# Optimization experiments

Measured on AMD Instinct MI355X. Metric: run time of the kernel, lower is better.

The kernel has to match this reference:

```python
import jax, jax.numpy as jnp
import numpy as np

N_QUBITS = 6
N_LAYERS = 2
QSVT_DEGREE = 3
DT_RANK = max(N_QUBITS // 2, 1)
OUT_DIM = 3 * N_QUBITS
PI = np.float32(np.pi)
DT_MIN, DT_MAX = 1e-3, 0.1
BATCH, SEQ = 256, 512


def _ry_mat(theta):
    c = jnp.cos(theta / 2)
    s = jnp.sin(theta / 2)
    row0 = jnp.stack([c, -s], axis=-1)
    row1 = jnp.stack([s, c], axis=-1)
    return jnp.stack([row0, row1], axis=-2).astype(jnp.complex64)


def _rz_mat(theta):
    e = jnp.exp(-0.5j * theta.astype(jnp.complex64))
    z = jnp.zeros_like(e)
    row0 = jnp.stack([e, z], axis=-1)
    row1 = jnp.stack([z, jnp.conj(e)], axis=-1)
    return jnp.stack([row0, row1], axis=-2)


def _rx_mat(theta):
    c = jnp.cos(theta / 2).astype(jnp.complex64)
    s = jnp.sin(theta / 2).astype(jnp.complex64)
    row0 = jnp.stack([c, -1j * s], axis=-1)
    row1 = jnp.stack([-1j * s, c], axis=-1)
    return jnp.stack([row0, row1], axis=-2)


def _apply1(state, mat, w):
    # state: (B, 2, ..., 2) tensor over N_QUBITS axes; mat: (2,2) or batched (B,2,2)
    state = jnp.moveaxis(state, 1 + w, -1)
    if mat.ndim == 3:
        state = jnp.einsum('bij,b...j->b...i', mat, state)
    else:
        state = jnp.einsum('ij,b...j->b...i', mat, state)
    return jnp.moveaxis(state, -1, 1 + w)


def _cnot(state, c, t):
    state = jnp.moveaxis(state, (1 + c, 1 + t), (-2, -1))
    state = state.at[..., 1, :].set(state[..., 1, ::-1])
    return jnp.moveaxis(state, (-2, -1), (1 + c, 1 + t))


def _crx(state, theta, c, t):
    state = jnp.moveaxis(state, (1 + c, 1 + t), (-2, -1))
    m = _rx_mat(theta)
    state = state.at[..., 1, :].set(jnp.einsum('ij,...j->...i', m, state[..., 1, :]))
    return jnp.moveaxis(state, (-2, -1), (1 + c, 1 + t))


def _circuit(h, x, dt, circuit_params, poly_coeffs, qsvt_params):
    """Batched statevector simulation of the selective QSVT + unified ansatz qnode."""
    n = N_QUBITS
    B = h.shape[0]
    state = jnp.zeros((B,) + (2,) * n, jnp.complex64)
    state = state.at[(slice(None),) + (0,) * n].set(1.0 + 0.0j)
    # 1) state encoding RY(h[t-1])
    for i in range(n):
        state = _apply1(state, _ry_mat(h[:, i]), i)
    # 2) Delta-modulated QSVT: RZ rotations + bidirectional CNOT ring per degree
    qidx = 0
    n_qp = n * QSVT_DEGREE
    for deg in range(QSVT_DEGREE + 1):
        coeff = poly_coeffs[deg]
        for i in range(n):
            if qidx < n_qp:
                ang = coeff * dt[:, i] * qsvt_params[qidx] * PI
                qidx += 1
            else:
                ang = coeff * dt[:, i] * PI
            state = _apply1(state, _rz_mat(ang), i)
        for i in range(n - 1):
            state = _cnot(state, i, i + 1)
        state = _cnot(state, n - 1, 0)
        for i in range(n - 1, 0, -1):
            state = _cnot(state, i, i - 1)
    # 3) unified variational ansatz
    p = 0
    for _ in range(N_LAYERS):
        for i in range(n):
            state = _apply1(state, _rx_mat(circuit_params[p]), i)
            state = _apply1(state, _ry_mat(circuit_params[p + 1]), i)
            state = _apply1(state, _rz_mat(circuit_params[p + 2]), i)
            p += 3
        for i in range(n):
            state = _crx(state, circuit_params[p], i, (i + 1) % n)
            p += 1
        for i in range(n - 1, -1, -1):
            state = _crx(state, circuit_params[p], i, (i - 1) % n)
            p += 1
    # 4) Delta-modulated input RY(x * dt)
    for i in range(n):
        state = _apply1(state, _ry_mat(x[:, i] * dt[:, i]), i)
    # 5) Pauli X/Y/Z expectation values per qubit
    xs, ys, zs = [], [], []
    for i in range(n):
        s = jnp.moveaxis(state, 1 + i, 1).reshape(B, 2, -1)
        z = jnp.sum(jnp.conj(s[:, 0]) * s[:, 1], axis=-1)
        xs.append(2.0 * jnp.real(z))
        ys.append(2.0 * jnp.imag(z))
        zs.append(jnp.sum(jnp.abs(s[:, 0]) ** 2 - jnp.abs(s[:, 1]) ** 2, axis=-1))
    return jnp.stack(xs + ys + zs, axis=-1).astype(jnp.float32)  # (B, 3n)


def setup_inputs() -> dict:
    key = jax.random.key(0)
    ks = jax.random.split(key, 8)
    angles = jax.random.uniform(ks[0], (BATCH, SEQ, N_QUBITS), jnp.float32) * PI
    Wx = jax.random.normal(ks[1], (DT_RANK + 2 * N_QUBITS, N_QUBITS), jnp.float32) / np.float32(np.sqrt(N_QUBITS))
    Wdt = jax.random.normal(ks[2], (N_QUBITS, DT_RANK), jnp.float32) / np.float32(np.sqrt(DT_RANK))
    dt = jnp.exp(jax.random.uniform(ks[3], (N_QUBITS,), jnp.float32) * np.float32(np.log(DT_MAX) - np.log(DT_MIN)) + np.float32(np.log(DT_MIN)))
    bdt = dt + jnp.log(-jnp.expm1(-dt))
    poly_coeffs = jax.random.normal(ks[4], (QSVT_DEGREE + 1,), jnp.float32) * 0.1
    qsvt_params = jax.random.normal(ks[5], (N_QUBITS * QSVT_DEGREE,), jnp.float32) * 0.1
    circuit_params = jax.random.normal(ks[6], (5 * N_QUBITS * N_LAYERS,), jnp.float32) * 0.1
    D = jnp.ones((OUT_DIM,), jnp.float32)
    Wc = jax.random.normal(ks[7], (OUT_DIM, N_QUBITS), jnp.float32) / np.float32(np.sqrt(N_QUBITS))
    return {"angles": angles, "Wx": Wx, "Wdt": Wdt, "bdt": bdt, "poly_coeffs": poly_coeffs, "qsvt_params": qsvt_params, "circuit_params": circuit_params, "D": D, "Wc": Wc}


def reference(angles, Wx, Wdt, bdt, poly_coeffs, qsvt_params, circuit_params, D, Wc):
    x_dbc = angles @ Wx.T  # (B,S, dt_rank + 2n)
    dt_raw = x_dbc[..., :DT_RANK]
    # B slice computed in the original but never used in forward
    C = x_dbc[..., DT_RANK + N_QUBITS:]
    dt_angles = jnp.tanh(jax.nn.softplus(dt_raw @ Wdt.T + bdt)) * PI  # (B,S,n)
    # quantum part is detached in the original (detach().cpu() before the qnode)
    sg = jax.lax.stop_gradient
    xs = (jnp.moveaxis(sg(angles), 1, 0), jnp.moveaxis(sg(dt_angles), 1, 0))
    cp, pc, qp = sg(circuit_params), sg(poly_coeffs), sg(qsvt_params)
    h0 = jnp.zeros((angles.shape[0], N_QUBITS), jnp.float32)

    def step(h, xt):
        x_t, dt_t = xt
        meas = _circuit(h, x_t, dt_t, cp, pc, qp)
        return meas[:, 2 * N_QUBITS:], meas  # carry = PauliZ block

    _, meas = jax.lax.scan(step, h0, xs)
    h_full = jnp.moveaxis(meas, 0, 1)  # (B,S,3n)
    return (C @ Wc.T) * h_full + D * jnp.concatenate([angles] * 3, axis=-1)
```

## Files before the change

kernel.cpp:

```cpp
#include <hip/hip_runtime.h>
#include <math.h>

#define BATCH 256
#define SEQ 512
#define SDS 54
#define PI_F 3.14159265358979323846f

template<int CTRL>
__device__ __forceinline__ float fdpp(float v) {
    return __int_as_float(__builtin_amdgcn_mov_dpp(__float_as_int(v), CTRL, 0xF, 0xF, true));
}
template<int L>
__device__ __forceinline__ float rdl(float v) {
    return __int_as_float(__builtin_amdgcn_readlane(__float_as_int(v), L));
}
__device__ __forceinline__ float rdlv(float v, int l) {
    return __int_as_float(__builtin_amdgcn_readlane(__float_as_int(v), l));
}
template<int M>
__device__ __forceinline__ float shxm(float v) {
    if constexpr (M == 1)       return fdpp<0xB1>(v);
    else if constexpr (M == 2)  return fdpp<0x4E>(v);
    else if constexpr (M == 8)  return fdpp<0x128>(v);
    else if constexpr (M == 32) return __shfl_xor(v, 32, 64);
    else return __int_as_float(__builtin_amdgcn_ds_swizzle(__float_as_int(v), (M << 10) | 0x1F));
}
__device__ __forceinline__ float redsum64(float v) {
    v += fdpp<0x128>(v);
    v += fdpp<0x124>(v);
    v += fdpp<0x122>(v);
    v += fdpp<0x121>(v);
    return (rdl<0>(v) + rdl<16>(v)) + (rdl<32>(v) + rdl<48>(v));
}
__device__ __forceinline__ float xorf(float v, int m) {
    return __int_as_float(__float_as_int(v) ^ m);
}
__device__ __forceinline__ void wg_barrier_lds() {
    __builtin_amdgcn_sched_barrier(0);
    __builtin_amdgcn_s_waitcnt(0xC07F);
    __builtin_amdgcn_s_barrier();
    __builtin_amdgcn_sched_barrier(0);
}
__device__ __forceinline__ int permf(int x) {
    const int cs[11] = {0,1,2,3,4,5,5,4,3,2,1};
    const int ts[11] = {1,2,3,4,5,0,4,3,2,1,0};
#pragma unroll
    for (int k = 10; k >= 0; k--) {
        int cb = (x >> (5 - cs[k])) & 1;
        x ^= cb << (5 - ts[k]);
    }
    return x;
}
__device__ __forceinline__ void cmul4(const float* c,
    float vr, float vi, float ar, float ai, float br, float bi, float cr, float ci,
    float& nr, float& ni) {
    nr = c[0]*vr - c[1]*vi + c[2]*ar - c[3]*ai + c[4]*br - c[5]*bi + c[6]*cr - c[7]*ci;
    ni = c[0]*vi + c[1]*vr + c[2]*ai + c[3]*ar + c[4]*bi + c[5]*br + c[6]*ci + c[7]*cr;
}
__device__ __forceinline__ void ringapply(const float* rc,
    float vr, float vi, float br, float bi, float cr, float ci, float dr, float di,
    float& nr, float& ni) {
    nr = rc[0]*vr - rc[1]*bi - rc[2]*ci + rc[3]*dr;
    ni = rc[0]*vi + rc[1]*br + rc[2]*cr + rc[3]*di;
}

__global__ __launch_bounds__(256) void prep_kernel(
    const float* __restrict__ angles, const float* __restrict__ Wx,
    const float* __restrict__ Wdt, const float* __restrict__ bdt,
    const float* __restrict__ D, const float* __restrict__ Wc,
    float* __restrict__ sd)
{
    int gid = blockIdx.x * blockDim.x + threadIdx.x;
    if (gid >= BATCH * SEQ) return;
    const float* a = angles + (size_t)gid * 6;
    float ang[6];
#pragma unroll
    for (int i = 0; i < 6; i++) ang[i] = a[i];
    float dtr[3];
#pragma unroll
    for (int r = 0; r < 3; r++) {
        float s = 0.f;
#pragma unroll
        for (int k = 0; k < 6; k++) s += ang[k] * Wx[r * 6 + k];
        dtr[r] = s;
    }
    float* rec = sd + (size_t)gid * SDS;
    float dtv[6];
#pragma unroll
    for (int i = 0; i < 6; i++) {
        float x = bdt[i];
#pragma unroll
        for (int r = 0; r < 3; r++) x += dtr[r] * Wdt[i * 3 + r];
        float sp = (x > 15.f) ? x : log1pf(expf(x));
        dtv[i] = tanhf(sp) * PI_F;
        rec[i] = dtv[i];
        float th = ang[i] * dtv[i];
        rec[6 + i]  = cosf(th);
        rec[12 + i] = sinf(th);
    }
    float C[6];
#pragma unroll
    for (int i = 0; i < 6; i++) {
        float s = 0.f;
#pragma unroll
        for (int k = 0; k < 6; k++) s += ang[k] * Wx[(9 + i) * 6 + k];
        C[i] = s;
    }
#pragma unroll
    for (int j = 0; j < 18; j++) {
        float s = 0.f;
#pragma unroll
        for (int i = 0; i < 6; i++) s += C[i] * Wc[j * 6 + i];
        rec[18 + j] = s;
        rec[36 + j] = D[j] * ang[j % 6];
    }
}

__global__ __launch_bounds__(64) void umat_kernel(const float* __restrict__ cp,
                                                  float2* __restrict__ um)
{
    const int lane = threadIdx.x;
    const int col = blockIdx.x;
    int bitv[6];
#pragma unroll
    for (int i = 0; i < 6; i++) bitv[i] = (lane >> (5 - i)) & 1;

    float qc[2][3][8], rc[2][6][4];
#pragma unroll
    for (int l = 0; l < 2; l++) {
        float g00r[6], g00i[6], g01r[6], g01i[6], g10r[6], g10i[6], g11r[6], g11i[6];
#pragma unroll
        for (int i = 0; i < 6; i++) {
            float ax = cp[l * 30 + i * 3 + 0];
            float ay = cp[l * 30 + i * 3 + 1];
            float az = cp[l * 30 + i * 3 + 2];
            float ca = cosf(0.5f * ax), sa = sinf(0.5f * ax);
            float cb = cosf(0.5f * ay), sb = sinf(0.5f * ay);
            float cg = cosf(0.5f * az), sg = sinf(0.5f * az);
            float m00r = cb * ca, m00i =  sb * sa;
            float m01r = -sb * ca, m01i = -cb * sa;
            float m10r =  sb * ca, m10i = -cb * sa;
            float m11r =  cb * ca, m11i = -sb * sa;
            g00r[i] = cg * m00r + sg * m00i; g00i[i] = cg * m00i - sg * m00r;
            g01r[i] = cg * m01r + sg * m01i; g01i[i] = cg * m01i - sg * m01r;
            g10r[i] = cg * m10r - sg * m10i; g10i[i] = cg * m10i + sg * m10r;
            g11r[i] = cg * m11r - sg * m11i; g11i[i] = cg * m11i + sg * m11r;
        }
#pragma unroll
        for (int pp = 0; pp < 3; pp++) {
            int aq = 2 * pp, bq = 2 * pp + 1;
            float dar = bitv[aq] ? g11r[aq] : g00r[aq], dai = bitv[aq] ? g11i[aq] : g00i[aq];
            float oar = bitv[aq] ? g10r[aq] : g01r[aq], oai = bitv[aq] ? g10i[aq] : g01i[aq];
            float dbr = bitv[bq] ? g11r[bq] : g00r[bq], dbi = bitv[bq] ? g11i[bq] : g00i[bq];
            float obr = bitv[bq] ? g10r[bq] : g01r[bq], obi = bitv[bq] ? g10i[bq] : g01i[bq];
            qc[l][pp][0] = dar * dbr - dai * dbi;  qc[l][pp][1] = dar * dbi + dai * dbr;
            qc[l][pp][2] = oar * dbr - oai * dbi;  qc[l][pp][3] = oar * dbi + oai * dbr;
            qc[l][pp][4] = dar * obr - dai * obi;  qc[l][pp][5] = dar * obi + dai * obr;
            qc[l][pp][6] = oar * obr - oai * obi;  qc[l][pp][7] = oar * obi + oai * obr;
        }
        const int Aq[6] = {0, 2, 4, 5, 3, 1};
        const int Bq[6] = {1, 3, 5, 4, 2, 0};
#pragma unroll
        for (int o = 0; o < 6; o++) {
            float tha = (o < 3) ? cp[l * 30 + 18 + 2 * o]     : cp[l * 30 + 24 + 2 * (o - 3)];
            float thb = (o < 3) ? cp[l * 30 + 18 + 2 * o + 1] : cp[l * 30 + 24 + 2 * (o - 3) + 1];
            float ca = cosf(0.5f * tha), sa = sinf(0.5f * tha);
            float cb = cosf(0.5f * thb), sb = sinf(0.5f * thb);
            int ba = bitv[Aq[o]], bb = bitv[Bq[o]];
            float mx0 = ba ? ca : 1.f, sae = ba ? sa : 0.f;
            float ny0 = bb ? cb : 1.f, sbe = bb ? sb : 0.f;
            rc[l][o][0] = ny0 * mx0; rc[l][o][1] = -ny0 * sae;
            rc[l][o][2] = -mx0 * sbe; rc[l][o][3] = -sae * sbe;
        }
    }

    float re = (lane == col) ? 1.f : 0.f;
    float im = 0.f;
    auto p1q = [&](int mi, int mj, const float* c) {
        float ar = __shfl_xor(re, mi, 64), ai = __shfl_xor(im, mi, 64);
        float br = __shfl_xor(re, mj, 64), bi = __shfl_xor(im, mj, 64);
        float cr = __shfl_xor(re, mi | mj, 64), ci = __shfl_xor(im, mi | mj, 64);
        float nr, ni;
        cmul4(c, re, im, ar, ai, br, bi, cr, ci, nr, ni);
        re = nr; im = ni;
    };
    auto rng = [&](int mb, int mc, const float* c) {
        float br = __shfl_xor(re, mb, 64), bi = __shfl_xor(im, mb, 64);
        float cr = __shfl_xor(re, mc, 64), ci = __shfl_xor(im, mc, 64);
        float dr = __shfl_xor(re, mb | mc, 64), di = __shfl_xor(im, mb | mc, 64);
        float nr, ni;
        ringapply(c, re, im, br, bi, cr, ci, dr, di, nr, ni);
        re = nr; im = ni;
    };
#pragma unroll
    for (int l = 0; l < 2; l++) {
        p1q(32, 16, qc[l][0]);
        p1q(8, 4, qc[l][1]);
        p1q(2, 1, qc[l][2]);
        rng(16, 8, rc[l][0]);
        rng(4, 2, rc[l][1]);
        rng(1, 32, rc[l][2]);
        rng(2, 4, rc[l][3]);
        rng(8, 16, rc[l][4]);
        rng(32, 1, rc[l][5]);
    }
    um[(size_t)lane * 64 + col] = make_float2(re, im);
}

__global__ __launch_bounds__(256, 1) void step_kernel(
    const float* __restrict__ sd, const float* __restrict__ pc,
    const float* __restrict__ qp, const float2* __restrict__ um,
    float* __restrict__ out)
{
    __shared__ float2 sPart[4][64];
    __shared__ __align__(16) float sZXY[20];
    const int tid = threadIdx.x;
    const int wave = tid >> 6;
    const int lane = tid & 63;
    const int b = blockIdx.x;

    int bitv[6];
#pragma unroll
    for (int i = 0; i < 6; i++) bitv[i] = (lane >> (5 - i)) & 1;
    int sflip[6];
#pragma unroll
    for (int q = 0; q < 6; q++) sflip[q] = bitv[q] ? (int)0x80000000 : 0;

    const int jbase = wave * 16;
    float2 row[16];
#pragma unroll
    for (int jj = 0; jj < 16; jj++) row[jj] = um[(size_t)lane * 64 + jbase + jj];

    float A[6], sel[6];
    {
        int x1 = permf(lane), x2 = permf(x1), x3 = permf(x2), x4 = permf(x3);
#pragma unroll
        for (int i = 0; i < 6; i++) {
            float u0 = pc[0] * PI_F * qp[0 * 6 + i];
            float u1 = pc[1] * PI_F * qp[1 * 6 + i];
            float u2 = pc[2] * PI_F * qp[2 * 6 + i];
            float u3 = pc[3] * PI_F;
            float t1 = ((x1 >> (5 - i)) & 1) ? 0.5f : -0.5f;
            float t2 = ((x2 >> (5 - i)) & 1) ? 0.5f : -0.5f;
            float t3 = ((x3 >> (5 - i)) & 1) ? 0.5f : -0.5f;
            float t4 = ((x4 >> (5 - i)) & 1) ? 0.5f : -0.5f;
            A[i] = u3 * t1 + u2 * t2 + u1 * t3 + u0 * t4;
            sel[i] = (float)((x4 >> (5 - i)) & 1);
        }
    }

    const float* sdb = sd + (size_t)b * SEQ * SDS;
    float* outb = out + (size_t)b * SEQ * 18;

    float h0 = 0.f, h1 = 0.f, h2 = 0.f, h3 = 0.f, h4 = 0.f, h5 = 0.f;

    float cd[18], nd[18];
#pragma unroll
    for (int k = 0; k < 18; k++) cd[k] = sdb[k];

    for (int t = 0; t < SEQ; t++) {
        const float* r  = sdb + (size_t)t * SDS;
        const float* rn = sdb + (size_t)((t + 1 < SEQ) ? t + 1 : t) * SDS;
#pragma unroll
        for (int k = 0; k < 18; k++) nd[k] = rn[k];

        float phi = A[0]*cd[0] + A[1]*cd[1] + A[2]*cd[2] + A[3]*cd[3] + A[4]*cd[4] + A[5]*cd[5];
        float sph, cph;
        __sincosf(phi, &sph, &cph);

        float ss0, cc0, ss1, cc1, ss2, cc2, ss3, cc3, ss4, cc4, ss5, cc5;
        __sincosf(0.5f * h0, &ss0, &cc0);
        __sincosf(0.5f * h1, &ss1, &cc1);
        __sincosf(0.5f * h2, &ss2, &cc2);
        __sincosf(0.5f * h3, &ss3, &cc3);
        __sincosf(0.5f * h4, &ss4, &cc4);
        __sincosf(0.5f * h5, &ss5, &cc5);
        float f0 = fmaf(sel[0], ss0 - cc0, cc0);
        float f1 = fmaf(sel[1], ss1 - cc1, cc1);
        float f2 = fmaf(sel[2], ss2 - cc2, cc2);
        float f3 = fmaf(sel[3], ss3 - cc3, cc3);
        float f4 = fmaf(sel[4], ss4 - cc4, cc4);
        float f5 = fmaf(sel[5], ss5 - cc5, cc5);
        float prod = ((f0 * f1) * (f2 * f3)) * (f4 * f5);
        float pr = prod * cph, pi = prod * sph;

        float ar0 = 0.f, ai0 = 0.f, ar1 = 0.f, ai1 = 0.f;
#pragma unroll
        for (int jj = 0; jj < 16; jj += 2) {
            float sr0 = rdlv(pr, jbase + jj);
            float si0 = rdlv(pi, jbase + jj);
            float sr1 = rdlv(pr, jbase + jj + 1);
            float si1 = rdlv(pi, jbase + jj + 1);
            ar0 = fmaf(row[jj].x, sr0, ar0);
            ar0 = fmaf(-row[jj].y, si0, ar0);
            ai0 = fmaf(row[jj].x, si0, ai0);
            ai0 = fmaf(row[jj].y, sr0, ai0);
            ar1 = fmaf(row[jj + 1].x, sr1, ar1);
            ar1 = fmaf(-row[jj + 1].y, si1, ar1);
            ai1 = fmaf(row[jj + 1].x, si1, ai1);
            ai1 = fmaf(row[jj + 1].y, sr1, ai1);
        }
        sPart[wave][lane] = make_float2(ar0 + ar1, ai0 + ai1);
        wg_barrier_lds();
        float2 q0v = sPart[0][lane], q1v = sPart[1][lane];
        float2 q2v = sPart[2][lane], q3v = sPart[3][lane];
        float re = (q0v.x + q1v.x) + (q2v.x + q3v.x);
        float im = (q0v.y + q1v.y) + (q2v.y + q3v.y);

        if (wave == 0) {
            float p = re * re + im * im;
            float Z0 = redsum64(xorf(p, sflip[0]));
            float Z1 = redsum64(xorf(p, sflip[1]));
            float Z2 = redsum64(xorf(p, sflip[2]));
            float Z3 = redsum64(xorf(p, sflip[3]));
            float Z4 = redsum64(xorf(p, sflip[4]));
            float Z5 = redsum64(xorf(p, sflip[5]));
            if (lane == 0) {
                sZXY[0] = Z0; sZXY[1] = Z1; sZXY[2] = Z2;
                sZXY[3] = Z3; sZXY[4] = Z4; sZXY[5] = Z5;
            }
        } else if (wave == 1) {
            float g0r = shxm<32>(re), g0i = shxm<32>(im);
            float g1r = shxm<16>(re), g1i = shxm<16>(im);
            float X0 = redsum64(re * g0r + im * g0i);
            float X1 = redsum64(re * g1r + im * g1i);
            float Y0 = redsum64(xorf(re * g0i - im * g0r, sflip[0]));
            float Y1 = redsum64(xorf(re * g1i - im * g1r, sflip[1]));
            if (lane == 0) { sZXY[6] = X0; sZXY[7] = X1; sZXY[12] = Y0; sZXY[13] = Y1; }
        } else if (wave == 2) {
            float g2r = shxm<8>(re), g2i = shxm<8>(im);
            float g3r = shxm<4>(re), g3i = shxm<4>(im);
            float X2 = redsum64(re * g2r + im * g2i);
            float X3 = redsum64(re * g3r + im * g3i);
            float Y2 = redsum64(xorf(re * g2i - im * g2r, sflip[2]));
            float Y3 = redsum64(xorf(re * g3i - im * g3r, sflip[3]));
            if (lane == 0) { sZXY[8] = X2; sZXY[9] = X3; sZXY[14] = Y2; sZXY[15] = Y3; }
        } else {
            float g4r = shxm<2>(re), g4i = shxm<2>(im);
            float g5r = shxm<1>(re), g5i = shxm<1>(im);
            float X4 = redsum64(re * g4r + im * g4i);
            float X5 = redsum64(re * g5r + im * g5i);
            float Y4 = redsum64(xorf(re * g4i - im * g4r, sflip[4]));
            float Y5 = redsum64(xorf(re * g5i - im * g5r, sflip[5]));
            if (lane == 0) { sZXY[10] = X4; sZXY[11] = X5; sZXY[16] = Y4; sZXY[17] = Y5; }
        }
        wg_barrier_lds();

        float4 v0 = ((const float4*)sZXY)[0];
        float4 v1 = ((const float4*)sZXY)[1];
        float4 v2 = ((const float4*)sZXY)[2];
        float Zv[6] = {v0.x, v0.y, v0.z, v0.w, v1.x, v1.y};
        float Xv[6] = {v1.z, v1.w, v2.x, v2.y, v2.z, v2.w};
        h0 = cd[6]  * Zv[0] - cd[12] * Xv[0];
        h1 = cd[7]  * Zv[1] - cd[13] * Xv[1];
        h2 = cd[8]  * Zv[2] - cd[14] * Xv[2];
        h3 = cd[9]  * Zv[3] - cd[15] * Xv[3];
        h4 = cd[10] * Zv[4] - cd[16] * Xv[4];
        h5 = cd[11] * Zv[5] - cd[17] * Xv[5];

        if (wave == 0 && lane == 0) {
            float* o = outb + (size_t)t * 18;
            float hh[6] = {h0, h1, h2, h3, h4, h5};
#pragma unroll
            for (int q = 0; q < 6; q++) o[12 + q] = fmaf(r[30 + q], hh[q], r[48 + q]);
        }
        if (wave == 3 && lane == 0) {
            float* o = outb + (size_t)t * 18;
#pragma unroll
            for (int q = 0; q < 6; q++) {
                float px = cd[6 + q] * Xv[q] + cd[12 + q] * Zv[q];
                o[q]     = fmaf(r[18 + q], px, r[36 + q]);
                o[6 + q] = fmaf(r[24 + q], sZXY[12 + q], r[42 + q]);
            }
        }

#pragma unroll
        for (int k = 0; k < 18; k++) cd[k] = nd[k];
    }
}

extern "C" void kernel_launch(void* const* d_in, const int* in_sizes, int n_in,
                              void* d_out, int out_size, void* d_ws, size_t ws_size,
                              hipStream_t stream) {
    const float* angles = (const float*)d_in[0];
    const float* Wx     = (const float*)d_in[1];
    const float* Wdt    = (const float*)d_in[2];
    const float* bdt    = (const float*)d_in[3];
    const float* pc     = (const float*)d_in[4];
    const float* qp     = (const float*)d_in[5];
    const float* cp     = (const float*)d_in[6];
    const float* D      = (const float*)d_in[7];
    const float* Wc     = (const float*)d_in[8];
    float* sd  = (float*)d_ws;
    float2* um = (float2*)(sd + (size_t)BATCH * SEQ * SDS);
    float* out = (float*)d_out;

    umat_kernel<<<64, 64, 0, stream>>>(cp, um);
    prep_kernel<<<(BATCH * SEQ) / 256, 256, 0, stream>>>(angles, Wx, Wdt, bdt, D, Wc, sd);
    step_kernel<<<BATCH, 256, 0, stream>>>(sd, pc, qp, um, out);
}
```

Before: 712.8 us.

## Compute Z/X reductions redundantly per wave to drop second barrier per step

Each of the four waves now computes all six Z and six X expectation reductions itself, so the LDS exchange of reduced values and the second workgroup barrier per timestep go away. The partial-sum buffer is double-buffered by step parity so one barrier per step stays safe. The Y reductions and X/Y output writes, which are off the recurrence's critical path, are deferred to wave 3 at the start of the next iteration. This trades more redundant cross-lane reduction work per wave for fewer barriers on the serial sequence loop.

New measurement: 801.7 us. 12.5% more time.

```diff
diff --git a/kernel.cpp b/kernel.cpp
--- a/kernel.cpp
+++ b/kernel.cpp
@@ -212,8 +212,7 @@
     const float* __restrict__ qp, const float2* __restrict__ um,
     float* __restrict__ out)
 {
-    __shared__ float2 sPart[4][64];
-    __shared__ __align__(16) float sZXY[20];
+    __shared__ float2 sPart[2][4][64];
     const int tid = threadIdx.x;
     const int wave = tid >> 6;
     const int lane = tid & 63;
@@ -253,6 +252,9 @@
     float* outb = out + (size_t)b * SEQ * 18;
 
     float h0 = 0.f, h1 = 0.f, h2 = 0.f, h3 = 0.f, h4 = 0.f, h5 = 0.f;
+    float ysv[6], pX[6];
+#pragma unroll
+    for (int q = 0; q < 6; q++) { ysv[q] = 0.f; pX[q] = 0.f; }
 
     float cd[18], nd[18];
 #pragma unroll
@@ -263,6 +265,21 @@
         const float* rn = sdb + (size_t)((t + 1 < SEQ) ? t + 1 : t) * SDS;
 #pragma unroll
         for (int k = 0; k < 18; k++) nd[k] = rn[k];
+
+        if (wave == 3 && t > 0) {
+            const float* rp = sdb + (size_t)(t - 1) * SDS;
+            float* o = outb + (size_t)(t - 1) * 18;
+            float Y0 = redsum64(ysv[0]), Y1 = redsum64(ysv[1]), Y2 = redsum64(ysv[2]);
+            float Y3 = redsum64(ysv[3]), Y4 = redsum64(ysv[4]), Y5 = redsum64(ysv[5]);
+            if (lane == 0) {
+                float Yv[6] = {Y0, Y1, Y2, Y3, Y4, Y5};
+#pragma unroll
+                for (int q = 0; q < 6; q++) {
+                    o[q]     = fmaf(rp[18 + q], pX[q], rp[36 + q]);
+                    o[6 + q] = fmaf(rp[24 + q], Yv[q], rp[42 + q]);
+                }
+            }
+        }
 
         float phi = A[0]*cd[0] + A[1]*cd[1] + A[2]*cd[2] + A[3]*cd[3] + A[4]*cd[4] + A[5]*cd[5];
         float sph, cph;
@@ -300,63 +317,40 @@
             ai1 = fmaf(row[jj + 1].x, si1, ai1);
             ai1 = fmaf(row[jj + 1].y, sr1, ai1);
         }
-        sPart[wave][lane] = make_float2(ar0 + ar1, ai0 + ai1);
+        sPart[t & 1][wave][lane] = make_float2(ar0 + ar1, ai0 + ai1);
         wg_barrier_lds();
-        float2 q0v = sPart[0][lane], q1v = sPart[1][lane];
-        float2 q2v = sPart[2][lane], q3v = sPart[3][lane];
+        float2 q0v = sPart[t & 1][0][lane], q1v = sPart[t & 1][1][lane];
+        float2 q2v = sPart[t & 1][2][lane], q3v = sPart[t & 1][3][lane];
         float re = (q0v.x + q1v.x) + (q2v.x + q3v.x);
         float im = (q0v.y + q1v.y) + (q2v.y + q3v.y);
 
-        if (wave == 0) {
-            float p = re * re + im * im;
-            float Z0 = redsum64(xorf(p, sflip[0]));
-            float Z1 = redsum64(xorf(p, sflip[1]));
-            float Z2 = redsum64(xorf(p, sflip[2]));
-            float Z3 = redsum64(xorf(p, sflip[3]));
-            float Z4 = redsum64(xorf(p, sflip[4]));
-            float Z5 = redsum64(xorf(p, sflip[5]));
-            if (lane == 0) {
-                sZXY[0] = Z0; sZXY[1] = Z1; sZXY[2] = Z2;
-                sZXY[3] = Z3; sZXY[4] = Z4; sZXY[5] = Z5;
-            }
-        } else if (wave == 1) {
-            float g0r = shxm<32>(re), g0i = shxm<32>(im);
-            float g1r = shxm<16>(re), g1i = shxm<16>(im);
-            float X0 = redsum64(re * g0r + im * g0i);
-            float X1 = redsum64(re * g1r + im * g1i);
-            float Y0 = redsum64(xorf(re * g0i - im * g0r, sflip[0]));
-            float Y1 = redsum64(xorf(re * g1i - im * g1r, sflip[1]));
-            if (lane == 0) { sZXY[6] = X0; sZXY[7] = X1; sZXY[12] = Y0; sZXY[13] = Y1; }
-        } else if (wave == 2) {
-            float g2r = shxm<8>(re), g2i = shxm<8>(im);
-            float g3r = shxm<4>(re), g3i = shxm<4>(im);
-            float X2 = redsum64(re * g2r + im * g2i);
-            float X3 = redsum64(re * g3r + im * g3i);
-            float Y2 = redsum64(xorf(re * g2i - im * g2r, sflip[2]));
-            float Y3 = redsum64(xorf(re * g3i - im * g3r, sflip[3]));
-            if (lane == 0) { sZXY[8] = X2; sZXY[9] = X3; sZXY[14] = Y2; sZXY[15] = Y3; }
-        } else {
-            float g4r = shxm<2>(re), g4i = shxm<2>(im);
-            float g5r = shxm<1>(re), g5i = shxm<1>(im);
-            float X4 = redsum64(re * g4r + im * g4i);
-            float X5 = redsum64(re * g5r + im * g5i);
-            float Y4 = redsum64(xorf(re * g4i - im * g4r, sflip[4]));
-            float Y5 = redsum64(xorf(re * g5i - im * g5r, sflip[5]));
-            if (lane == 0) { sZXY[10] = X4; sZXY[11] = X5; sZXY[16] = Y4; sZXY[17] = Y5; }
-        }
-        wg_barrier_lds();
-
-        float4 v0 = ((const float4*)sZXY)[0];
-        float4 v1 = ((const float4*)sZXY)[1];
-        float4 v2 = ((const float4*)sZXY)[2];
-        float Zv[6] = {v0.x, v0.y, v0.z, v0.w, v1.x, v1.y};
-        float Xv[6] = {v1.z, v1.w, v2.x, v2.y, v2.z, v2.w};
-        h0 = cd[6]  * Zv[0] - cd[12] * Xv[0];
-        h1 = cd[7]  * Zv[1] - cd[13] * Xv[1];
-        h2 = cd[8]  * Zv[2] - cd[14] * Xv[2];
-        h3 = cd[9]  * Zv[3] - cd[15] * Xv[3];
-        h4 = cd[10] * Zv[4] - cd[16] * Xv[4];
-        h5 = cd[11] * Zv[5] - cd[17] * Xv[5];
+        float p = re * re + im * im;
+        float g0r = shxm<32>(re), g0i = shxm<32>(im);
+        float g1r = shxm<16>(re), g1i = shxm<16>(im);
+        float g2r = shxm<8>(re),  g2i = shxm<8>(im);
+        float g3r = shxm<4>(re),  g3i = shxm<4>(im);
+        float g4r = shxm<2>(re),  g4i = shxm<2>(im);
+        float g5r = shxm<1>(re),  g5i = shxm<1>(im);
+
+        float Z0 = redsum64(xorf(p, sflip[0]));
+        float Z1 = redsum64(xorf(p, sflip[1]));
+        float Z2 = redsum64(xorf(p, sflip[2]));
+        float Z3 = redsum64(xorf(p, sflip[3]));
+        float Z4 = redsum64(xorf(p, sflip[4]));
+        float Z5 = redsum64(xorf(p, sflip[5]));
+        float X0 = redsum64(fmaf(re, g0r, im * g0i));
+        float X1 = redsum64(fmaf(re, g1r, im * g1i));
+        float X2 = redsum64(fmaf(re, g2r, im * g2i));
+        float X3 = redsum64(fmaf(re, g3r, im * g3i));
+        float X4 = redsum64(fmaf(re, g4r, im * g4i));
+        float X5 = redsum64(fmaf(re, g5r, im * g5i));
+
+        h0 = cd[6]  * Z0 - cd[12] * X0;
+        h1 = cd[7]  * Z1 - cd[13] * X1;
+        h2 = cd[8]  * Z2 - cd[14] * X2;
+        h3 = cd[9]  * Z3 - cd[15] * X3;
+        h4 = cd[10] * Z4 - cd[16] * X4;
+        h5 = cd[11] * Z5 - cd[17] * X5;
 
         if (wave == 0 && lane == 0) {
             float* o = outb + (size_t)t * 18;
@@ -364,18 +358,36 @@
 #pragma unroll
             for (int q = 0; q < 6; q++) o[12 + q] = fmaf(r[30 + q], hh[q], r[48 + q]);
         }
-        if (wave == 3 && lane == 0) {
-            float* o = outb + (size_t)t * 18;
+        if (wave == 3) {
+            ysv[0] = xorf(re * g0i - im * g0r, sflip[0]);
+            ysv[1] = xorf(re * g1i - im * g1r, sflip[1]);
+            ysv[2] = xorf(re * g2i - im * g2r, sflip[2]);
+            ysv[3] = xorf(re * g3i - im * g3r, sflip[3]);
+            ysv[4] = xorf(re * g4i - im * g4r, sflip[4]);
+            ysv[5] = xorf(re * g5i - im * g5r, sflip[5]);
+            float Zv[6] = {Z0, Z1, Z2, Z3, Z4, Z5};
+            float Xv[6] = {X0, X1, X2, X3, X4, X5};
+#pragma unroll
+            for (int q = 0; q < 6; q++) pX[q] = cd[6 + q] * Xv[q] + cd[12 + q] * Zv[q];
+        }
+
+#pragma unroll
+        for (int k = 0; k < 18; k++) cd[k] = nd[k];
+    }
+
+    if (wave == 3) {
+        const float* rp = sdb + (size_t)(SEQ - 1) * SDS;
+        float* o = outb + (size_t)(SEQ - 1) * 18;
+        float Y0 = redsum64(ysv[0]), Y1 = redsum64(ysv[1]), Y2 = redsum64(ysv[2]);
+        float Y3 = redsum64(ysv[3]), Y4 = redsum64(ysv[4]), Y5 = redsum64(ysv[5]);
+        if (lane == 0) {
+            float Yv[6] = {Y0, Y1, Y2, Y3, Y4, Y5};
 #pragma unroll
             for (int q = 0; q < 6; q++) {
-                float px = cd[6 + q] * Xv[q] + cd[12 + q] * Zv[q];
-                o[q]     = fmaf(r[18 + q], px, r[36 + q]);
-                o[6 + q] = fmaf(r[24 + q], sZXY[12 + q], r[42 + q]);
+                o[q]     = fmaf(rp[18 + q], pX[q], rp[36 + q]);
+                o[6 + q] = fmaf(rp[24 + q], Yv[q], rp[42 + q]);
             }
         }
-
-#pragma unroll
-        for (int k = 0; k < 18; k++) cd[k] = nd[k];
     }
 }
 
```

## Split step kernel across eight waves with double-buffered partials and native sincos

Applied to the files above, without the earlier changes.

Doubles the workgroup from 4 to 8 waves, so each wave handles 8 columns of the unitary matvec and the Z/X/Y reductions are spread over more waves. The partial-sum LDS buffer is double-buffered by timestep parity, output scale/offset values are prefetched one step ahead into registers by the storing waves, and sincos uses the hardware sin/cos instructions on pre-scaled arguments. The goal is to shorten the serial per-timestep critical path. In exchange, each barrier now synchronizes 8 waves, and the native sin/cos may be less accurate for large arguments.

Measured after the change: 837.1 us. 17.4% more time.

```diff
diff --git a/kernel.cpp b/kernel.cpp
--- a/kernel.cpp
+++ b/kernel.cpp
@@ -5,6 +5,7 @@
 #define SEQ 512
 #define SDS 54
 #define PI_F 3.14159265358979323846f
+#define INV2PI 0.15915494309189535f
 
 template<int CTRL>
 __device__ __forceinline__ float fdpp(float v) {
@@ -34,6 +35,11 @@
 }
 __device__ __forceinline__ float xorf(float v, int m) {
     return __int_as_float(__float_as_int(v) ^ m);
+}
+__device__ __forceinline__ void nsincos(float x, float& s, float& c) {
+    float r = x * INV2PI;
+    s = __builtin_amdgcn_sinf(r);
+    c = __builtin_amdgcn_cosf(r);
 }
 __device__ __forceinline__ void wg_barrier_lds() {
     __builtin_amdgcn_sched_barrier(0);
@@ -207,13 +213,14 @@
     um[(size_t)lane * 64 + col] = make_float2(re, im);
 }
 
-__global__ __launch_bounds__(256, 1) void step_kernel(
+__global__ __launch_bounds__(512, 2) void step_kernel(
     const float* __restrict__ sd, const float* __restrict__ pc,
     const float* __restrict__ qp, const float2* __restrict__ um,
     float* __restrict__ out)
 {
-    __shared__ float2 sPart[4][64];
-    __shared__ __align__(16) float sZXY[20];
+    __shared__ float2 sPart[2][8][64];
+    __shared__ __align__(16) float sZX[12];
+    __shared__ float sY[6];
     const int tid = threadIdx.x;
     const int wave = tid >> 6;
     const int lane = tid & 63;
@@ -226,10 +233,10 @@
 #pragma unroll
     for (int q = 0; q < 6; q++) sflip[q] = bitv[q] ? (int)0x80000000 : 0;
 
-    const int jbase = wave * 16;
-    float2 row[16];
-#pragma unroll
-    for (int jj = 0; jj < 16; jj++) row[jj] = um[(size_t)lane * 64 + jbase + jj];
+    const int jbase = wave * 8;
+    float2 row[8];
+#pragma unroll
+    for (int jj = 0; jj < 8; jj++) row[jj] = um[(size_t)lane * 64 + jbase + jj];
 
     float A[6], sel[6];
     {
@@ -252,29 +259,40 @@
     const float* sdb = sd + (size_t)b * SEQ * SDS;
     float* outb = out + (size_t)b * SEQ * 18;
 
+    const bool isStorer = (wave == 0 || wave == 6 || wave == 7);
+    const int sb1 = (wave == 0) ? 30 : (wave == 6) ? 18 : 24;
+    const int sb2 = (wave == 0) ? 48 : (wave == 6) ? 36 : 42;
+
     float h0 = 0.f, h1 = 0.f, h2 = 0.f, h3 = 0.f, h4 = 0.f, h5 = 0.f;
 
-    float cd[18], nd[18];
+    float cd[18], nd[18], sf[12], sfn[12];
 #pragma unroll
     for (int k = 0; k < 18; k++) cd[k] = sdb[k];
+    if (isStorer) {
+#pragma unroll
+        for (int j = 0; j < 6; j++) { sf[j] = sdb[sb1 + j]; sf[6 + j] = sdb[sb2 + j]; }
+    }
 
     for (int t = 0; t < SEQ; t++) {
-        const float* r  = sdb + (size_t)t * SDS;
         const float* rn = sdb + (size_t)((t + 1 < SEQ) ? t + 1 : t) * SDS;
 #pragma unroll
         for (int k = 0; k < 18; k++) nd[k] = rn[k];
+        if (isStorer) {
+#pragma unroll
+            for (int j = 0; j < 6; j++) { sfn[j] = rn[sb1 + j]; sfn[6 + j] = rn[sb2 + j]; }
+        }
 
         float phi = A[0]*cd[0] + A[1]*cd[1] + A[2]*cd[2] + A[3]*cd[3] + A[4]*cd[4] + A[5]*cd[5];
         float sph, cph;
-        __sincosf(phi, &sph, &cph);
+        nsincos(phi, sph, cph);
 
         float ss0, cc0, ss1, cc1, ss2, cc2, ss3, cc3, ss4, cc4, ss5, cc5;
-        __sincosf(0.5f * h0, &ss0, &cc0);
-        __sincosf(0.5f * h1, &ss1, &cc1);
-        __sincosf(0.5f * h2, &ss2, &cc2);
-        __sincosf(0.5f * h3, &ss3, &cc3);
-        __sincosf(0.5f * h4, &ss4, &cc4);
-        __sincosf(0.5f * h5, &ss5, &cc5);
+        nsincos(0.5f * h0, ss0, cc0);
+        nsincos(0.5f * h1, ss1, cc1);
+        nsincos(0.5f * h2, ss2, cc2);
+        nsincos(0.5f * h3, ss3, cc3);
+        nsincos(0.5f * h4, ss4, cc4);
+        nsincos(0.5f * h5, ss5, cc5);
         float f0 = fmaf(sel[0], ss0 - cc0, cc0);
         float f1 = fmaf(sel[1], ss1 - cc1, cc1);
         float f2 = fmaf(sel[2], ss2 - cc2, cc2);
@@ -286,7 +304,7 @@
 
         float ar0 = 0.f, ai0 = 0.f, ar1 = 0.f, ai1 = 0.f;
 #pragma unroll
-        for (int jj = 0; jj < 16; jj += 2) {
+        for (int jj = 0; jj < 8; jj += 2) {
             float sr0 = rdlv(pr, jbase + jj);
             float si0 = rdlv(pi, jbase + jj);
             float sr1 = rdlv(pr, jbase + jj + 1);
@@ -300,55 +318,64 @@
             ai1 = fmaf(row[jj + 1].x, si1, ai1);
             ai1 = fmaf(row[jj + 1].y, sr1, ai1);
         }
-        sPart[wave][lane] = make_float2(ar0 + ar1, ai0 + ai1);
+        sPart[t & 1][wave][lane] = make_float2(ar0 + ar1, ai0 + ai1);
         wg_barrier_lds();
-        float2 q0v = sPart[0][lane], q1v = sPart[1][lane];
-        float2 q2v = sPart[2][lane], q3v = sPart[3][lane];
-        float re = (q0v.x + q1v.x) + (q2v.x + q3v.x);
-        float im = (q0v.y + q1v.y) + (q2v.y + q3v.y);
-
-        if (wave == 0) {
+        float re, im;
+        {
+            float2 v0 = sPart[t & 1][0][lane], v1 = sPart[t & 1][1][lane];
+            float2 v2 = sPart[t & 1][2][lane], v3 = sPart[t & 1][3][lane];
+            float2 v4 = sPart[t & 1][4][lane], v5 = sPart[t & 1][5][lane];
+            float2 v6 = sPart[t & 1][6][lane], v7 = sPart[t & 1][7][lane];
+            re = ((v0.x + v1.x) + (v2.x + v3.x)) + ((v4.x + v5.x) + (v6.x + v7.x));
+            im = ((v0.y + v1.y) + (v2.y + v3.y)) + ((v4.y + v5.y) + (v6.y + v7.y));
+        }
+
+        if (wave < 3) {
             float p = re * re + im * im;
-            float Z0 = redsum64(xorf(p, sflip[0]));
-            float Z1 = redsum64(xorf(p, sflip[1]));
-            float Z2 = redsum64(xorf(p, sflip[2]));
-            float Z3 = redsum64(xorf(p, sflip[3]));
-            float Z4 = redsum64(xorf(p, sflip[4]));
-            float Z5 = redsum64(xorf(p, sflip[5]));
-            if (lane == 0) {
-                sZXY[0] = Z0; sZXY[1] = Z1; sZXY[2] = Z2;
-                sZXY[3] = Z3; sZXY[4] = Z4; sZXY[5] = Z5;
-            }
-        } else if (wave == 1) {
+            int q0 = 2 * wave, q1 = 2 * wave + 1;
+            float Za = redsum64(xorf(p, sflip[q0]));
+            float Zb = redsum64(xorf(p, sflip[q1]));
+            if (lane == 0) { sZX[q0] = Za; sZX[q1] = Zb; }
+        } else if (wave == 3) {
             float g0r = shxm<32>(re), g0i = shxm<32>(im);
             float g1r = shxm<16>(re), g1i = shxm<16>(im);
-            float X0 = redsum64(re * g0r + im * g0i);
-            float X1 = redsum64(re * g1r + im * g1i);
+            float X0 = redsum64(fmaf(re, g0r, im * g0i));
+            float X1 = redsum64(fmaf(re, g1r, im * g1i));
+            if (lane == 0) { sZX[6] = X0; sZX[7] = X1; }
+        } else if (wave == 4) {
+            float g2r = shxm<8>(re), g2i = shxm<8>(im);
+            float g3r = shxm<4>(re), g3i = shxm<4>(im);
+            float X2 = redsum64(fmaf(re, g2r, im * g2i));
+            float X3 = redsum64(fmaf(re, g3r, im * g3i));
+            if (lane == 0) { sZX[8] = X2; sZX[9] = X3; }
+        } else if (wave == 5) {
+            float g4r = shxm<2>(re), g4i = shxm<2>(im);
+            float g5r = shxm<1>(re), g5i = shxm<1>(im);
+            float X4 = redsum64(fmaf(re, g4r, im * g4i));
+            float X5 = redsum64(fmaf(re, g5r, im * g5i));
+            if (lane == 0) { sZX[10] = X4; sZX[11] = X5; }
+        } else if (wave == 6) {
+            float g0r = shxm<32>(re), g0i = shxm<32>(im);
+            float g1r = shxm<16>(re), g1i = shxm<16>(im);
+            float g2r = shxm<8>(re),  g2i = shxm<8>(im);
             float Y0 = redsum64(xorf(re * g0i - im * g0r, sflip[0]));
             float Y1 = redsum64(xorf(re * g1i - im * g1r, sflip[1]));
-            if (lane == 0) { sZXY[6] = X0; sZXY[7] = X1; sZXY[12] = Y0; sZXY[13] = Y1; }
-        } else if (wave == 2) {
-            float g2r = shxm<8>(re), g2i = shxm<8>(im);
+            float Y2 = redsum64(xorf(re * g2i - im * g2r, sflip[2]));
+            if (lane == 0) { sY[0] = Y0; sY[1] = Y1; sY[2] = Y2; }
+        } else {
             float g3r = shxm<4>(re), g3i = shxm<4>(im);
-            float X2 = redsum64(re * g2r + im * g2i);
-            float X3 = redsum64(re * g3r + im * g3i);
-            float Y2 = redsum64(xorf(re * g2i - im * g2r, sflip[2]));
-            float Y3 = redsum64(xorf(re * g3i - im * g3r, sflip[3]));
-            if (lane == 0) { sZXY[8] = X2; sZXY[9] = X3; sZXY[14] = Y2; sZXY[15] = Y3; }
-        } else {
             float g4r = shxm<2>(re), g4i = shxm<2>(im);
             float g5r = shxm<1>(re), g5i = shxm<1>(im);
-            float X4 = redsum64(re * g4r + im * g4i);
-            float X5 = redsum64(re * g5r + im * g5i);
+            float Y3 = redsum64(xorf(re * g3i - im * g3r, sflip[3]));
             float Y4 = redsum64(xorf(re * g4i - im * g4r, sflip[4]));
             float Y5 = redsum64(xorf(re * g5i - im * g5r, sflip[5]));
-            if (lane == 0) { sZXY[10] = X4; sZXY[11] = X5; sZXY[16] = Y4; sZXY[17] = Y5; }
+            if (lane == 0) { sY[3] = Y3; sY[4] = Y4; sY[5] = Y5; }
         }
         wg_barrier_lds();
 
-        float4 v0 = ((const float4*)sZXY)[0];
-        float4 v1 = ((const float4*)sZXY)[1];
-        float4 v2 = ((const float4*)sZXY)[2];
+        float4 v0 = ((const float4*)sZX)[0];
+        float4 v1 = ((const float4*)sZX)[1];
+        float4 v2 = ((const float4*)sZX)[2];
         float Zv[6] = {v0.x, v0.y, v0.z, v0.w, v1.x, v1.y};
         float Xv[6] = {v1.z, v1.w, v2.x, v2.y, v2.z, v2.w};
         h0 = cd[6]  * Zv[0] - cd[12] * Xv[0];
@@ -358,24 +385,30 @@
         h4 = cd[10] * Zv[4] - cd[16] * Xv[4];
         h5 = cd[11] * Zv[5] - cd[17] * Xv[5];
 
-        if (wave == 0 && lane == 0) {
+        if (lane == 0) {
             float* o = outb + (size_t)t * 18;
-            float hh[6] = {h0, h1, h2, h3, h4, h5};
-#pragma unroll
-            for (int q = 0; q < 6; q++) o[12 + q] = fmaf(r[30 + q], hh[q], r[48 + q]);
-        }
-        if (wave == 3 && lane == 0) {
-            float* o = outb + (size_t)t * 18;
-#pragma unroll
-            for (int q = 0; q < 6; q++) {
-                float px = cd[6 + q] * Xv[q] + cd[12 + q] * Zv[q];
-                o[q]     = fmaf(r[18 + q], px, r[36 + q]);
-                o[6 + q] = fmaf(r[24 + q], sZXY[12 + q], r[42 + q]);
+            if (wave == 0) {
+                float hh[6] = {h0, h1, h2, h3, h4, h5};
+#pragma unroll
+                for (int q = 0; q < 6; q++) o[12 + q] = fmaf(sf[q], hh[q], sf[6 + q]);
+            } else if (wave == 6) {
+#pragma unroll
+                for (int q = 0; q < 6; q++) {
+                    float px = cd[6 + q] * Xv[q] + cd[12 + q] * Zv[q];
+                    o[q] = fmaf(sf[q], px, sf[6 + q]);
+                }
+            } else if (wave == 7) {
+#pragma unroll
+                for (int q = 0; q < 6; q++) o[6 + q] = fmaf(sf[q], sY[q], sf[6 + q]);
             }
         }
 
 #pragma unroll
         for (int k = 0; k < 18; k++) cd[k] = nd[k];
+        if (isStorer) {
+#pragma unroll
+            for (int k = 0; k < 12; k++) sf[k] = sfn[k];
+        }
     }
 }
 
@@ -397,5 +430,5 @@
 
     umat_kernel<<<64, 64, 0, stream>>>(cp, um);
     prep_kernel<<<(BATCH * SEQ) / 256, 256, 0, stream>>>(angles, Wx, Wdt, bdt, D, Wc, sd);
-    step_kernel<<<BATCH, 256, 0, stream>>>(sd, pc, qp, um, out);
-}
+    step_kernel<<<BATCH, 512, 0, stream>>>(sd, pc, qp, um, out);
+}
```
